# Kernel tuning notes

Measured on AMD Instinct MI355X. Metric: run time of the kernel, lower is better.

The kernel has to match this reference:

```python
import jax, jax.numpy as jnp
import numpy as np

H = 512      # hidden_size
GH = 512     # global_hidden_size
V = 128      # VOCAB_SIZE (one-hot arg_hot width)
D = 14       # tree depth; complete binary tree
NUM_OPS = 36
N_INT = 5    # num_internal_ops
N_NODES = 2 ** (D + 1) - 1  # 32767, heap layout: node i has children 2i+1, 2i+2


def _p(key, i, shape, s=0.05):
    return jax.random.normal(jax.random.fold_in(key, i), shape, dtype=jnp.float32) * s


def setup_inputs() -> dict:
    key = jax.random.key(0)
    return {
        "tokens": jax.random.randint(jax.random.fold_in(key, 0), (N_NODES,), 0, V),
        "validity_mask": jnp.ones((NUM_OPS,), jnp.float32),
        # binary tree-LSTM (blstm): 2 children
        "W_iou_b": _p(key, 1, (V, 3 * H)), "U_iou_b": _p(key, 2, (2, H, 3 * H)), "b_iou_b": jnp.zeros((3 * H,), jnp.float32),
        "Wf_b": _p(key, 3, (V, H)), "Uf_b": _p(key, 4, (2, H, H)), "bf_b": jnp.ones((H,), jnp.float32),
        # ternary tree-LSTM (tlstm): 3 children
        "W_iou_t": _p(key, 5, (V, 3 * H)), "U_iou_t": _p(key, 6, (3, H, 3 * H)), "b_iou_t": jnp.zeros((3 * H,), jnp.float32),
        "Wf_t": _p(key, 7, (V, H)), "Uf_t": _p(key, 8, (3, H, H)), "bf_t": jnp.ones((H,), jnp.float32),
        # FFN: one h-by-h layer (ffn_complexity = h^2 * n_layers, n_layers=1)
        "ffn_W": _p(key, 9, (H, H)), "ffn_b": jnp.zeros((H,), jnp.float32),
        # global LSTM (1 layer, 1 step), torch gate order i,f,g,o
        "lstm_Wx": _p(key, 10, (H, 4 * GH)), "lstm_Wh": _p(key, 11, (GH, 4 * GH)), "lstm_b": jnp.zeros((4 * GH,), jnp.float32),
        # actor heads on concat(root_hidden, h_glob)
        "hl_W": _p(key, 12, (H + GH, 2)), "hl_b": jnp.zeros((2,), jnp.float32),
        "int_W": _p(key, 13, (H + GH, N_INT)), "int_b": jnp.zeros((N_INT,), jnp.float32),
        "act_W": _p(key, 14, (H + GH, NUM_OPS)), "act_b": jnp.zeros((NUM_OPS,), jnp.float32),
    }


def _nary_cell(x, hk, ck, W_iou, U_iou, b_iou, Wf, Uf, bf):
    # x: [n, V]; hk, ck: [n, K, H]  (K children)
    iou = x @ W_iou + jnp.einsum('nkh,khg->ng', hk, U_iou) + b_iou
    i, o, u = jnp.split(iou, 3, axis=-1)
    f = jax.nn.sigmoid((x @ Wf + bf)[:, None, :] + jnp.einsum('nkh,khg->nkg', hk, Uf))
    c = jax.nn.sigmoid(i) * jnp.tanh(u) + jnp.sum(f * ck, axis=1)
    h = jax.nn.sigmoid(o) * jnp.tanh(c)
    return h, c


def _forward(tokens, validity_mask, W_iou_b, U_iou_b, b_iou_b, Wf_b, Uf_b, bf_b,
             W_iou_t, U_iou_t, b_iou_t, Wf_t, Uf_t, bf_t, ffn_W, ffn_b,
             lstm_Wx, lstm_Wh, lstm_b, hl_W, hl_b, int_W, int_b, act_W, act_b):
    arg_hot = jax.nn.one_hot(tokens, V, dtype=jnp.float32)  # [N_NODES, V]
    h_prev = c_prev = None
    h_ab = c_ab = None
    # apply_binary_lstm over the whole tree, bottom-up, one batched cell per level
    for lvl in range(D, -1, -1):
        n = 2 ** lvl
        x = arg_hot[n - 1:2 * n - 1]  # level lvl occupies heap slots [2^l-1, 2^{l+1}-2]
        if h_prev is None:
            hk = jnp.zeros((n, 2, H), jnp.float32)  # leaves: tz children
            ck = hk
        else:
            hk = h_prev.reshape(n, 2, H)
            ck = c_prev.reshape(n, 2, H)
        h_prev, c_prev = _nary_cell(x, hk, ck, W_iou_b, U_iou_b, b_iou_b, Wf_b, Uf_b, bf_b)
        if lvl == 1:
            h_ab, c_ab = h_prev, c_prev  # root's children a, b
    # apply_ternary_lstm at depth 0: children = (self.hidden, a.hidden, b.hidden)
    hk3 = jnp.concatenate([h_prev, h_ab], axis=0)[None]  # [1, 3, H]
    ck3 = jnp.concatenate([c_prev, c_ab], axis=0)[None]
    h_root, c_root = _nary_cell(arg_hot[0:1], hk3, ck3, W_iou_t, U_iou_t, b_iou_t, Wf_t, Uf_t, bf_t)
    # apply_ffn (1 layer) then apply_global_lstm (single step from zero state)
    h_f = jnp.maximum(h_root @ ffn_W + ffn_b, 0.0)  # [1, H]
    h_g = jnp.zeros((1, GH), jnp.float32)
    c_g = h_g
    gates = h_f @ lstm_Wx + h_g @ lstm_Wh + lstm_b
    gi, gf, gg, go = jnp.split(gates, 4, axis=-1)
    c_g = jax.nn.sigmoid(gf) * c_g + jax.nn.sigmoid(gi) * jnp.tanh(gg)
    h_g = jax.nn.sigmoid(go) * jnp.tanh(c_g)
    # actor heads
    feat = jnp.concatenate([h_f, h_g], axis=-1)  # [1, H+GH]
    hl = feat @ hl_W + hl_b
    il = feat @ int_W + int_b
    el = jnp.log(validity_mask)[None, :] + feat @ (act_W * validity_mask[None, :]) + act_b * validity_mask
    return jnp.concatenate([hl, il, el], axis=-1)  # [1, 2 + N_INT + NUM_OPS]


def reference(tokens, validity_mask, W_iou_b, U_iou_b, b_iou_b, Wf_b, Uf_b, bf_b,
              W_iou_t, U_iou_t, b_iou_t, Wf_t, Uf_t, bf_t, ffn_W, ffn_b,
              lstm_Wx, lstm_Wh, lstm_b, hl_W, hl_b, int_W, int_b, act_W, act_b):
    return _forward(tokens, validity_mask, W_iou_b, U_iou_b, b_iou_b, Wf_b, Uf_b, bf_b,
                    W_iou_t, U_iou_t, b_iou_t, Wf_t, Uf_t, bf_t, ffn_W, ffn_b,
                    lstm_Wx, lstm_Wh, lstm_b, hl_W, hl_b, int_W, int_b, act_W, act_b)
```

## Files before the change

### kernel.cpp

```cpp
#include <hip/hip_runtime.h>
#include <hip/hip_bf16.h>
#include <math.h>

#define H 512
#define V 128
#define NLEAF 16384

typedef __attribute__((ext_vector_type(4))) float f32x4;
typedef __attribute__((ext_vector_type(8))) short s16x8;
typedef __attribute__((ext_vector_type(4))) unsigned short u16x4;
typedef unsigned short ushort_t;

__device__ ushort_t g_hb0[NLEAF * H];
__device__ ushort_t g_hb1[(NLEAF / 2) * H];
__device__ float    g_c0[NLEAF * H];
__device__ float    g_c1[(NLEAF / 2) * H];
__device__ __align__(16) ushort_t g_htab[V * H];
__device__ __align__(16) float    g_ctab[V * H];
__device__ __align__(16) float    g_Wpack[V * H * 4];
__device__ __align__(16) float    g_Uh0[V * 3 * H];
__device__ __align__(16) float    g_Uh1[V * 3 * H];
__device__ __align__(16) float    g_Vf0[V * H];
__device__ __align__(16) float    g_Vf1[V * H];
__device__ __align__(16) float    g_uhp[4 * 2 * V * 2048];
__device__ ushort_t g_UiouT[3 * H * 2 * H];
__device__ ushort_t g_UfT[H * 2 * H];
__device__ ushort_t g_UiouTt[3 * H * 3 * H];
__device__ ushort_t g_UfTt[H * 3 * H];
__device__ float    g_rpart[3 * 3072];
__device__ float    g_hf[H];
__device__ float    g_gates[4 * H];

__device__ __forceinline__ float sigm(float x) { return 1.0f / (1.0f + __expf(-x)); }
__device__ __forceinline__ float ftanh(float x) {
  return 1.0f - 2.0f / (__expf(2.0f * x) + 1.0f);
}
__device__ __forceinline__ ushort_t f2bf(float x) {
  __hip_bfloat16 b = __float2bfloat16(x);
  return *reinterpret_cast<ushort_t*>(&b);
}
__device__ __forceinline__ float bf2f(ushort_t u) {
  union { unsigned int i; float f; } v; v.i = ((unsigned int)u) << 16; return v.f;
}
__device__ __forceinline__ void gload_lds16(const void* g, void* l) {
  __builtin_amdgcn_global_load_lds(
      (const __attribute__((address_space(1))) unsigned int*)g,
      (__attribute__((address_space(3))) unsigned int*)l, 16, 0, 0);
}
#define WAITV(N) asm volatile("s_waitcnt vmcnt(" #N ")" ::: "memory")

__global__ __launch_bounds__(256) void k_prep(
    const float* __restrict__ s0, const float* __restrict__ s1,
    const float* __restrict__ s2, const float* __restrict__ s3,
    ushort_t* __restrict__ d0, ushort_t* __restrict__ d1,
    ushort_t* __restrict__ d2, ushort_t* __restrict__ d3,
    const float* __restrict__ Wiou, const float* __restrict__ biou,
    const float* __restrict__ Wf, const float* __restrict__ bf) {
  if (blockIdx.z == 4) {
    const int v = blockIdx.y * 48 + blockIdx.x;
    if (v >= V) return;
    for (int j = threadIdx.x; j < H; j += 256) {
      float wi = Wiou[(size_t)v * 1536 + j] + biou[j];
      float wo = Wiou[(size_t)v * 1536 + 512 + j] + biou[512 + j];
      float wu = Wiou[(size_t)v * 1536 + 1024 + j] + biou[1024 + j];
      float wf = Wf[(size_t)v * 512 + j] + bf[j];
      f32x4 wp = {wi, wo, wu, wf};
      *reinterpret_cast<f32x4*>(&g_Wpack[((size_t)v * 512 + j) * 4]) = wp;
      float c = sigm(wi) * ftanh(wu);
      float h = sigm(wo) * ftanh(c);
      g_htab[v * H + j] = f2bf(h);
      g_ctab[v * H + j] = c;
    }
    return;
  }
  const float* src; ushort_t* dst; int R, Cc;
  switch (blockIdx.z) {
    case 0: src = s0; dst = d0; R = 1024; Cc = 1536; break;
    case 1: src = s1; dst = d1; R = 1024; Cc = 512; break;
    case 2: src = s2; dst = d2; R = 1536; Cc = 1536; break;
    default: src = s3; dst = d3; R = 1536; Cc = 512; break;
  }
  int bc = blockIdx.x * 32, br = blockIdx.y * 32;
  if (bc >= Cc || br >= R) return;
  __shared__ float t[32][33];
  int tx = threadIdx.x & 31, ty = threadIdx.x >> 5;
  for (int rr = ty; rr < 32; rr += 8)
    t[rr][tx] = src[(size_t)(br + rr) * Cc + bc + tx];
  __syncthreads();
  for (int rr = ty; rr < 32; rr += 8)
    dst[(size_t)(bc + rr) * R + br + tx] = f2bf(t[tx][rr]);
}

__global__ __launch_bounds__(256) void k_uhg() {
  const int cb0 = blockIdx.x * 64;
  const int kh = blockIdx.y;
  const int kc = blockIdx.z;
  const int tid = threadIdx.x;
  const int lane = tid & 63;
  const int w = tid >> 6;
  const int wry = w >> 1;
  const int cx = w & 1;

  __shared__ f32x4 suv[3072];
  char* smem = (char*)suv;

  const unsigned kA = (unsigned)(kc * 256) + ((lane >> 4) * 16);
  const unsigned kB = (unsigned)(kh * 1024) + kA;
  #pragma unroll
  for (int uu = 0; uu < 3; ++uu) {
    int u = w * 3 + uu;
    const char* base;
    unsigned dstb;
    if (u < 8) {
      int row = u * 16 + (lane & 15);
      base = (const char*)g_htab + (size_t)row * 1024 + kA;
      dstb = (unsigned)u * 4096u;
    } else {
      int col = cb0 + (u - 8) * 16 + (lane & 15);
      const ushort_t* cp = (col < 1536) ? (g_UiouT + (size_t)col * 1024)
                                        : (g_UfT + (size_t)(col - 1536) * 1024);
      base = (const char*)cp + kB;
      dstb = 32768u + (unsigned)(u - 8) * 4096u;
    }
    #pragma unroll
    for (int kt = 0; kt < 4; ++kt)
      gload_lds16(base + kt * 64, smem + dstb + kt * 1024u);
  }
  WAITV(0);
  __syncthreads();

  f32x4 acc[4][2];
  #pragma unroll
  for (int a = 0; a < 4; ++a) { acc[a][0] = (f32x4){0,0,0,0}; acc[a][1] = (f32x4){0,0,0,0}; }

  #pragma unroll
  for (int kt = 0; kt < 4; ++kt) {
    const char* ab = smem + wry * 16384 + kt * 1024 + lane * 16;
    const char* bb = smem + 32768 + cx * 8192 + kt * 1024 + lane * 16;
    s16x8 b0 = *(const s16x8*)(bb);
    s16x8 b1 = *(const s16x8*)(bb + 4096);
    #pragma unroll
    for (int rtl = 0; rtl < 4; ++rtl) {
      s16x8 av = *(const s16x8*)(ab + rtl * 4096);
      acc[rtl][0] = __builtin_amdgcn_mfma_f32_16x16x32_bf16(av, b0, acc[rtl][0], 0, 0, 0);
      acc[rtl][1] = __builtin_amdgcn_mfma_f32_16x16x32_bf16(av, b1, acc[rtl][1], 0, 0, 0);
    }
  }

  float* outb = g_uhp + ((size_t)(kc * 2 + kh) * V) * 2048;
  #pragma unroll
  for (int rtl = 0; rtl < 4; ++rtl) {
    #pragma unroll
    for (int t = 0; t < 2; ++t) {
      int col = cb0 + cx * 32 + t * 16 + (lane & 15);
      int vb = wry * 64 + rtl * 16 + (lane >> 4) * 4;
      #pragma unroll
      for (int r = 0; r < 4; ++r)
        outb[(size_t)(vb + r) * 2048 + col] = acc[rtl][t][r];
    }
  }
}

__global__ __launch_bounds__(256) void k_uhred() {
  int e = blockIdx.x * 256 + threadIdx.x;
  float s = g_uhp[e] + g_uhp[524288 + e] + g_uhp[2 * 524288 + e]
          + g_uhp[3 * 524288 + e];
  int kh = e >> 18;
  int rem = e & 262143;
  int v = rem >> 11;
  int c = rem & 2047;
  if (c < 1536) (kh ? g_Uh1 : g_Uh0)[(size_t)v * 1536 + c] = s;
  else          (kh ? g_Vf1 : g_Vf0)[(size_t)v * 512 + (c - 1536)] = s;
}

__global__ __launch_bounds__(256) void k_top_cell(const int* __restrict__ tokens) {
  const int total = 8192 * 128;
  for (int q = blockIdx.x * 256 + threadIdx.x; q < total; q += gridDim.x * 256) {
    int i = q >> 7, jv = q & 127;
    int t0 = tokens[(NLEAF - 1) + 2 * i];
    int t1 = tokens[(NLEAF - 1) + 2 * i + 1];
    int tk = tokens[8191 + i];
    const f32x4* u0 = (const f32x4*)&g_Uh0[(size_t)t0 * 1536];
    const f32x4* u1 = (const f32x4*)&g_Uh1[(size_t)t1 * 1536];
    f32x4 ii = u0[jv] + u1[jv];
    f32x4 oo = u0[128 + jv] + u1[128 + jv];
    f32x4 uu = u0[256 + jv] + u1[256 + jv];
    f32x4 v0 = ((const f32x4*)&g_Vf0[(size_t)t0 * 512])[jv];
    f32x4 v1 = ((const f32x4*)&g_Vf1[(size_t)t1 * 512])[jv];
    f32x4 c0 = ((const f32x4*)&g_ctab[(size_t)t0 * 512])[jv];
    f32x4 c1 = ((const f32x4*)&g_ctab[(size_t)t1 * 512])[jv];
    const f32x4* wpp = (const f32x4*)g_Wpack + (size_t)tk * 512 + jv * 4;
    u16x4 hv; f32x4 cv;
    #pragma unroll
    for (int r = 0; r < 4; ++r) {
      f32x4 wp = wpp[r];
      float ig = ii[r] + wp[0];
      float og = oo[r] + wp[1];
      float ug = uu[r] + wp[2];
      float fp = wp[3];
      float cc = sigm(ig) * ftanh(ug) + sigm(fp + v0[r]) * c0[r]
               + sigm(fp + v1[r]) * c1[r];
      float hh = sigm(og) * ftanh(cc);
      cv[r] = cc;
      hv[r] = f2bf(hh);
    }
    *reinterpret_cast<u16x4*>(&g_hb1[(size_t)q * 4]) = hv;
    *reinterpret_cast<f32x4*>(&g_c1[(size_t)q * 4]) = cv;
  }
}

#define COMPUTE64(FA, S)                                                     \
  {                                                                          \
    const char* ab = smem + buf * 16384 + wry * 8192 + (S) * 1024 + lane * 16; \
    s16x8 a0 = *(const s16x8*)(ab);                                          \
    s16x8 a1 = *(const s16x8*)(ab + 2048);                                   \
    s16x8 a2 = *(const s16x8*)(ab + 4096);                                   \
    s16x8 a3 = *(const s16x8*)(ab + 6144);                                   \
    const char* bb = smem + 32768 + buf * 32768 + cx * 4096 + (S) * 1024 + lane * 16; \
    s16x8 b0 = *(const s16x8*)(bb);                                          \
    s16x8 b1 = *(const s16x8*)(bb + 2048);                                   \
    s16x8 b2 = *(const s16x8*)(bb + 8192);                                   \
    s16x8 b3 = *(const s16x8*)(bb + 10240);                                  \
    s16x8 b4 = *(const s16x8*)(bb + 16384);                                  \
    s16x8 b5 = *(const s16x8*)(bb + 18432);                                  \
    s16x8 b6 = *(const s16x8*)(bb + 24576);                                  \
    s16x8 b7 = *(const s16x8*)(bb + 26624);                                  \
    s16x8 aa[4] = {a0, a1, a2, a3};                                          \
    _Pragma("unroll")                                                        \
    for (int rtl = 0; rtl < 4; ++rtl) {                                      \
      acc[rtl][0] = __builtin_amdgcn_mfma_f32_16x16x32_bf16(aa[rtl], b0, acc[rtl][0], 0, 0, 0); \
      acc[rtl][1] = __builtin_amdgcn_mfma_f32_16x16x32_bf16(aa[rtl], b1, acc[rtl][1], 0, 0, 0); \
      acc[rtl][2] = __builtin_amdgcn_mfma_f32_16x16x32_bf16(aa[rtl], b2, acc[rtl][2], 0, 0, 0); \
      acc[rtl][3] = __builtin_amdgcn_mfma_f32_16x16x32_bf16(aa[rtl], b3, acc[rtl][3], 0, 0, 0); \
      acc[rtl][4] = __builtin_amdgcn_mfma_f32_16x16x32_bf16(aa[rtl], b4, acc[rtl][4], 0, 0, 0); \
      acc[rtl][5] = __builtin_amdgcn_mfma_f32_16x16x32_bf16(aa[rtl], b5, acc[rtl][5], 0, 0, 0); \
      acc[rtl][FA] = __builtin_amdgcn_mfma_f32_16x16x32_bf16(aa[rtl], b6, acc[rtl][FA], 0, 0, 0); \
      acc[rtl][FA + 1] = __builtin_amdgcn_mfma_f32_16x16x32_bf16(aa[rtl], b7, acc[rtl][FA + 1], 0, 0, 0); \
    }                                                                        \
  }

__global__ __launch_bounds__(256, 1) void k_mfma_rest(int lvl,
    const int* __restrict__ tokens) {
  const int n = 1 << lvl;
  const int node0 = n - 1;
  const int outp = lvl & 1;
  const ushort_t* __restrict__ hprev = outp ? g_hb0 : g_hb1;
  const float* __restrict__ cprev = outp ? g_c0 : g_c1;
  ushort_t* __restrict__ hout = outp ? g_hb1 : g_hb0;
  float* __restrict__ cout = outp ? g_c1 : g_c0;

  const int i0 = blockIdx.x * 128;
  const int j0 = blockIdx.y * 64;
  const int tid = threadIdx.x;
  const int lane = tid & 63;
  const int w = tid >> 6;
  const int wry = w >> 1;
  const int cx = w & 1;

  __shared__ f32x4 smemv[6144];
  char* smem = (char*)smemv;

  const char* gp[6];
  unsigned lb[6], lstr[6];
  {
    int kb = (lane >> 4) * 16;
    #pragma unroll
    for (int q = 0; q < 6; ++q) {
      int c = w * 6 + q;
      if (c < 8) {
        int row = i0 + c * 16 + (lane & 15);
        gp[q] = (const char*)hprev + (size_t)row * 2048 + kb;
        lb[q] = c * 2048u;
        lstr[q] = 16384u;
      } else {
        int ct = c - 8;
        int col = ct * 16 + (lane & 15);
        int g = col >> 6, jj = j0 + (col & 63);
        const ushort_t* Ub = (g < 3) ? (g_UiouT + (size_t)(g * 512 + jj) * 1024)
                                     : (g_UfT + (size_t)jj * 1024);
        gp[q] = (const char*)Ub + kb;
        lb[q] = 32768u + ct * 2048u;
        lstr[q] = 32768u;
      }
    }
  }

#define STAGE2(BUF)                                                          \
  {                                                                          \
    _Pragma("unroll")                                                        \
    for (int q = 0; q < 6; ++q) {                                            \
      gload_lds16(gp[q], smem + lb[q] + (unsigned)(BUF) * lstr[q]);          \
      gp[q] += 64;                                                           \
      gload_lds16(gp[q], smem + lb[q] + (unsigned)(BUF) * lstr[q] + 1024u);  \
      gp[q] += 64;                                                           \
    }                                                                        \
  }

  f32x4 acc[4][10];
  #pragma unroll
  for (int a = 0; a < 4; ++a)
    #pragma unroll
    for (int b = 0; b < 10; ++b) acc[a][b] = (f32x4){0.f, 0.f, 0.f, 0.f};

  STAGE2(0); STAGE2(1);
  int buf = 0;
  for (int ph = 0; ph < 8; ++ph) {
    WAITV(12);
    __builtin_amdgcn_s_barrier();
    COMPUTE64(6, 0);
    COMPUTE64(6, 1);
    __builtin_amdgcn_s_barrier();
    STAGE2(buf);
    buf ^= 1;
  }
  for (int ph = 8; ph < 14; ++ph) {
    WAITV(12);
    __builtin_amdgcn_s_barrier();
    COMPUTE64(8, 0);
    COMPUTE64(8, 1);
    __builtin_amdgcn_s_barrier();
    STAGE2(buf);
    buf ^= 1;
  }
  WAITV(12); __builtin_amdgcn_s_barrier();
  COMPUTE64(8, 0); COMPUTE64(8, 1);
  buf ^= 1;
  WAITV(0); __builtin_amdgcn_s_barrier();
  COMPUTE64(8, 0); COMPUTE64(8, 1);
#undef STAGE2

  const int node_c = lane >> 4;
  const int jl = lane & 15;
  #pragma unroll
  for (int t = 0; t < 2; ++t) {
    const int j = j0 + cx * 32 + t * 16 + jl;
    #pragma unroll
    for (int rtl = 0; rtl < 4; ++rtl) {
      f32x4 vi = acc[rtl][0 + t], vo = acc[rtl][2 + t], vu = acc[rtl][4 + t],
            v0 = acc[rtl][6 + t], v1 = acc[rtl][8 + t];
      const int ib = i0 + wry * 64 + rtl * 16 + node_c * 4;
      #pragma unroll
      for (int r = 0; r < 4; ++r) {
        int i = ib + r;
        int tok = tokens[node0 + i];
        f32x4 wp = ((const f32x4*)g_Wpack)[(size_t)tok * 512 + j];
        float ig = vi[r] + wp[0];
        float og = vo[r] + wp[1];
        float ug = vu[r] + wp[2];
        float fpre = wp[3];
        float cc = sigm(ig) * ftanh(ug)
                 + sigm(fpre + v0[r]) * cprev[(size_t)(2 * i) * 512 + j]
                 + sigm(fpre + v1[r]) * cprev[(size_t)(2 * i + 1) * 512 + j];
        float hh = sigm(og) * ftanh(cc);
        hout[(size_t)i * 512 + j] = f2bf(hh);
        cout[(size_t)i * 512 + j] = cc;
      }
    }
  }
}

__global__ __launch_bounds__(256) void k_small(int lvl,
    const int* __restrict__ tokens) {
  const int n = 1 << lvl;
  const int node0 = n - 1;
  const int outp = lvl & 1;
  const ushort_t* __restrict__ hprev = outp ? g_hb0 : g_hb1;
  const float* __restrict__ cprev = outp ? g_c0 : g_c1;
  ushort_t* __restrict__ hout = outp ? g_hb1 : g_hb0;
  float* __restrict__ cout = outp ? g_c1 : g_c0;

  const int i = blockIdx.y;
  const int j0 = blockIdx.x * 64;
  const int tid = threadIdx.x;
  const int g = tid >> 6;
  const int jc = tid & 63;
  const int jj = j0 + jc;

  __shared__ float hl[1024];
  __shared__ float exch[5][64];
  for (int t = tid; t < 1024; t += 256) hl[t] = bf2f(hprev[(size_t)i * 1024 + t]);
  __syncthreads();

  const ushort_t* col = (g < 3) ? (g_UiouT + (size_t)(g * 512 + jj) * 1024)
                                : (g_UfT + (size_t)jj * 1024);
  float a0 = 0.f, a1 = 0.f;
  #pragma unroll 4
  for (int k0 = 0; k0 < 512; k0 += 8) {
    s16x8 wv = *(const s16x8*)(col + k0);
    #pragma unroll
    for (int r = 0; r < 8; ++r) a0 += hl[k0 + r] * bf2f((ushort_t)wv[r]);
  }
  #pragma unroll 4
  for (int k0 = 512; k0 < 1024; k0 += 8) {
    s16x8 wv = *(const s16x8*)(col + k0);
    #pragma unroll
    for (int r = 0; r < 8; ++r) a1 += hl[k0 + r] * bf2f((ushort_t)wv[r]);
  }
  if (g < 3) exch[g][jc] = a0 + a1;
  else { exch[3][jc] = a0; exch[4][jc] = a1; }
  __syncthreads();

  if (tid < 64) {
    int j = j0 + tid;
    int tok = tokens[node0 + i];
    f32x4 wp = ((const f32x4*)g_Wpack)[(size_t)tok * 512 + j];
    float ig = exch[0][tid] + wp[0];
    float og = exch[1][tid] + wp[1];
    float ug = exch[2][tid] + wp[2];
    float fpre = wp[3];
    float cc = sigm(ig) * ftanh(ug)
             + sigm(fpre + exch[3][tid]) * cprev[(size_t)(2 * i) * 512 + j]
             + sigm(fpre + exch[4][tid]) * cprev[(size_t)(2 * i + 1) * 512 + j];
    float hh = sigm(og) * ftanh(cc);
    hout[(size_t)i * 512 + j] = f2bf(hh);
    cout[(size_t)i * 512 + j] = cc;
  }
}

__global__ __launch_bounds__(256) void k_root_p1() {
  const int by = blockIdx.y;
  const int tid = threadIdx.x;
  const int c = blockIdx.x * 256 + tid;

  __shared__ float hl[512];
  {
    int m0 = by * 512;
    #pragma unroll
    for (int q = 0; q < 2; ++q) {
      int t = tid + q * 256, m = m0 + t;
      hl[t] = (m < 512) ? bf2f(g_hb0[m]) : bf2f(g_hb1[m - 512]);
    }
  }
  __syncthreads();

  float acc = 0.f;
  const ushort_t* col = nullptr;
  if (c < 1536) {
    col = g_UiouTt + (size_t)c * 1536 + by * 512;
  } else {
    int v = c - 1536;
    if ((v >> 9) == by) col = g_UfTt + (size_t)(v & 511) * 1536 + by * 512;
  }
  if (col) {
    #pragma unroll 4
    for (int k0 = 0; k0 < 512; k0 += 8) {
      s16x8 wv = *(const s16x8*)(col + k0);
      #pragma unroll
      for (int r = 0; r < 8; ++r) acc += hl[k0 + r] * bf2f((ushort_t)wv[r]);
    }
  }
  g_rpart[(size_t)by * 3072 + c] = acc;
}

__global__ __launch_bounds__(512) void k_p2h1(const int* __restrict__ tokens,
    const float* __restrict__ Wiou_t, const float* __restrict__ biou_t,
    const float* __restrict__ Wf_t, const float* __restrict__ bf_t,
    const float* __restrict__ ffnW, const float* __restrict__ ffnb) {
  __shared__ float hroot[H];
  const int j = threadIdx.x;
  float ai = g_rpart[j] + g_rpart[3072 + j] + g_rpart[6144 + j];
  float ao = g_rpart[512 + j] + g_rpart[3072 + 512 + j] + g_rpart[6144 + 512 + j];
  float au = g_rpart[1024 + j] + g_rpart[3072 + 1024 + j] + g_rpart[6144 + 1024 + j];
  float f0 = g_rpart[1536 + j] + g_rpart[3072 + 1536 + j] + g_rpart[6144 + 1536 + j];
  float f1 = g_rpart[2048 + j] + g_rpart[3072 + 2048 + j] + g_rpart[6144 + 2048 + j];
  float f2 = g_rpart[2560 + j] + g_rpart[3072 + 2560 + j] + g_rpart[6144 + 2560 + j];

  int tok = tokens[0];
  float fpre = Wf_t[(size_t)tok * H + j] + bf_t[j];
  float ig = ai + Wiou_t[(size_t)tok * 3 * H + j] + biou_t[j];
  float og = ao + Wiou_t[(size_t)tok * 3 * H + H + j] + biou_t[H + j];
  float ug = au + Wiou_t[(size_t)tok * 3 * H + 2 * H + j] + biou_t[2 * H + j];
  float cc = sigm(ig) * ftanh(ug)
           + sigm(fpre + f0) * g_c0[j]
           + sigm(fpre + f1) * g_c1[j]
           + sigm(fpre + f2) * g_c1[H + j];
  hroot[j] = sigm(og) * ftanh(cc);
  __syncthreads();

  float acc = ffnb[j];
  #pragma unroll 8
  for (int m = 0; m < H; ++m) acc += hroot[m] * ffnW[m * H + j];
  g_hf[j] = fmaxf(acc, 0.0f);
}

__global__ __launch_bounds__(64) void k_head2(const float* __restrict__ Wx,
                                              const float* __restrict__ lb) {
  int idx = blockIdx.x * 64 + threadIdx.x;
  int region = idx >> 9;
  int j = idx & 511;
  int g2 = (region == 0) ? j : ((region == 1) ? 1024 + j : 1536 + j);
  float acc = lb[g2];
  #pragma unroll 8
  for (int m = 0; m < H; ++m) acc += g_hf[m] * Wx[m * 4 * H + g2];
  g_gates[g2] = acc;
}

__global__ __launch_bounds__(512) void k_head3(const float* __restrict__ vm,
    const float* __restrict__ hlW, const float* __restrict__ hlb,
    const float* __restrict__ intW, const float* __restrict__ intb,
    const float* __restrict__ actW, const float* __restrict__ actb,
    float* __restrict__ out) {
  __shared__ float feat[2 * H];
  int j = threadIdx.x;
  float ci = sigm(g_gates[j]) * ftanh(g_gates[2 * H + j]);
  float hg = sigm(g_gates[3 * H + j]) * ftanh(ci);
  feat[j] = g_hf[j];
  feat[H + j] = hg;
  __syncthreads();

  const int wv = threadIdx.x >> 6;
  const int lane = threadIdx.x & 63;
  for (int o = wv; o < 43; o += 8) {
    const float* Wc;
    int stride, colb;
    if (o < 2)       { Wc = hlW;  stride = 2;  colb = o; }
    else if (o < 7)  { Wc = intW; stride = 5;  colb = o - 2; }
    else             { Wc = actW; stride = 36; colb = o - 7; }
    float s = 0.f;
    #pragma unroll
    for (int q = 0; q < 16; ++q) {
      int m = lane + q * 64;
      s += feat[m] * Wc[(size_t)m * stride + colb];
    }
    #pragma unroll
    for (int d = 32; d >= 1; d >>= 1) s += __shfl_xor(s, d);
    if (lane == 0) {
      float res;
      if (o < 2)      res = s + hlb[o];
      else if (o < 7) res = s + intb[o - 2];
      else {
        int a = o - 7;
        float v = vm[a];
        res = __logf(v) + s * v + actb[a] * v;
      }
      out[o] = res;
    }
  }
}

extern "C" void kernel_launch(void* const* d_in, const int* in_sizes, int n_in,
                              void* d_out, int out_size, void* d_ws, size_t ws_size,
                              hipStream_t stream) {
  (void)in_sizes; (void)n_in; (void)d_ws; (void)ws_size; (void)out_size;
  const int* tokens   = (const int*)d_in[0];
  const float* vm     = (const float*)d_in[1];
  const float* Wiou_b = (const float*)d_in[2];
  const float* Uiou_b = (const float*)d_in[3];
  const float* biou_b = (const float*)d_in[4];
  const float* Wf_b   = (const float*)d_in[5];
  const float* Uf_b   = (const float*)d_in[6];
  const float* bf_b   = (const float*)d_in[7];
  const float* Wiou_t = (const float*)d_in[8];
  const float* Uiou_t = (const float*)d_in[9];
  const float* biou_t = (const float*)d_in[10];
  const float* Wf_t   = (const float*)d_in[11];
  const float* Uf_t   = (const float*)d_in[12];
  const float* bf_t   = (const float*)d_in[13];
  const float* ffnW   = (const float*)d_in[14];
  const float* ffnb   = (const float*)d_in[15];
  const float* lstmWx = (const float*)d_in[16];
  const float* lstmb  = (const float*)d_in[18];
  const float* hlW    = (const float*)d_in[19];
  const float* hlb    = (const float*)d_in[20];
  const float* intW   = (const float*)d_in[21];
  const float* intb   = (const float*)d_in[22];
  const float* actW   = (const float*)d_in[23];
  const float* actb   = (const float*)d_in[24];

  ushort_t* UiouT;  hipGetSymbolAddress((void**)&UiouT, HIP_SYMBOL(g_UiouT));
  ushort_t* UfT;    hipGetSymbolAddress((void**)&UfT, HIP_SYMBOL(g_UfT));
  ushort_t* UiouTt; hipGetSymbolAddress((void**)&UiouTt, HIP_SYMBOL(g_UiouTt));
  ushort_t* UfTt;   hipGetSymbolAddress((void**)&UfTt, HIP_SYMBOL(g_UfTt));

  k_prep<<<dim3(48, 48, 5), 256, 0, stream>>>(
      Uiou_b, Uf_b, Uiou_t, Uf_t, UiouT, UfT, UiouTt, UfTt,
      Wiou_b, biou_b, Wf_b, bf_b);

  k_uhg<<<dim3(32, 2, 4), 256, 0, stream>>>();
  k_uhred<<<2048, 256, 0, stream>>>();
  k_top_cell<<<2048, 256, 0, stream>>>(tokens);

  for (int lvl = 12; lvl >= 8; --lvl) {
    int gx = (1 << lvl) / 128;
    k_mfma_rest<<<dim3(gx, 8), 256, 0, stream>>>(lvl, tokens);
  }
  for (int lvl = 7; lvl >= 0; --lvl) {
    int n = 1 << lvl;
    k_small<<<dim3(8, n), 256, 0, stream>>>(lvl, tokens);
  }
  k_root_p1<<<dim3(12, 3), 256, 0, stream>>>();
  k_p2h1<<<1, 512, 0, stream>>>(tokens, Wiou_t, biou_t, Wf_t, bf_t, ffnW, ffnb);
  k_head2<<<24, 64, 0, stream>>>(lstmWx, lstmb);
  k_head3<<<1, 512, 0, stream>>>(vm, hlW, hlb, intW, intb, actW, actb, (float*)d_out);
}
```

Baseline: 607.6 us.

## Pre-pack U weights into MFMA staging layout and use wave-per-column GEMV reductions

Adds a k_packU kernel that converts the binary-cell U matrices to bf16 in a tile-contiguous layout matching the MFMA level kernel's LDS staging order. Each wave then reads contiguous 1 KB chunks instead of strided rows. k_small and k_root_p1 now assign one wave per output column, keep the hidden vector in registers, use coalesced 16-byte weight loads, and reduce with cross-lane shuffles, replacing per-thread column walks over shared memory. The cost is an extra prep launch and a larger global scratch buffer.

```diff
diff --git a/kernel.cpp b/kernel.cpp
--- a/kernel.cpp
+++ b/kernel.cpp
@@ -25,6 +25,7 @@
 __device__ __align__(16) float    g_uhp[4 * 2 * V * 2048];
 __device__ ushort_t g_UiouT[3 * H * 2 * H];
 __device__ ushort_t g_UfT[H * 2 * H];
+__device__ __align__(16) ushort_t g_Ustage[8 * 16 * 32 * 64 * 8];
 __device__ ushort_t g_UiouTt[3 * H * 3 * H];
 __device__ ushort_t g_UfTt[H * 3 * H];
 __device__ float    g_rpart[3 * 3072];
@@ -89,6 +90,31 @@
   __syncthreads();
   for (int rr = ty; rr < 32; rr += 8)
     dst[(size_t)(bc + rr) * R + br + tx] = f2bf(t[tx][rr]);
+}
+
+__global__ __launch_bounds__(256) void k_packU(const float* __restrict__ Uiou,
+                                               const float* __restrict__ Uf) {
+  const int jb = blockIdx.x;
+  const int ct = blockIdx.y;
+  const int kz = blockIdx.z;
+  const int t = threadIdx.x;
+  const int kt = kz * 4 + (t >> 6);
+  const int lane = t & 63;
+  const int colu = ct * 16 + (lane & 15);
+  const int g = colu >> 6;
+  const int jj = jb * 64 + (colu & 63);
+  const int kbase = kt * 32 + ((lane >> 4) << 3);
+  u16x4 v0, v1;
+  #pragma unroll
+  for (int r = 0; r < 8; ++r) {
+    int k = kbase + r;
+    float v = (g < 3) ? Uiou[(size_t)k * 1536 + g * 512 + jj]
+                      : Uf[(size_t)k * 512 + jj];
+    if (r < 4) v0[r] = f2bf(v); else v1[r - 4] = f2bf(v);
+  }
+  ushort_t* dst = g_Ustage + (((size_t)(jb * 16 + ct) * 32 + kt) * 64 + lane) * 8;
+  *reinterpret_cast<u16x4*>(dst) = v0;
+  *reinterpret_cast<u16x4*>(dst + 4) = v1;
 }
 
 __global__ __launch_bounds__(256) void k_uhg() {
@@ -261,7 +287,7 @@
   char* smem = (char*)smemv;
 
   const char* gp[6];
-  unsigned lb[6], lstr[6];
+  unsigned lb[6], lstr[6], off2[6], adv[6];
   {
     int kb = (lane >> 4) * 16;
     #pragma unroll
@@ -270,17 +296,13 @@
       if (c < 8) {
         int row = i0 + c * 16 + (lane & 15);
         gp[q] = (const char*)hprev + (size_t)row * 2048 + kb;
-        lb[q] = c * 2048u;
-        lstr[q] = 16384u;
+        lb[q] = c * 2048u; lstr[q] = 16384u; off2[q] = 64u; adv[q] = 128u;
       } else {
         int ct = c - 8;
-        int col = ct * 16 + (lane & 15);
-        int g = col >> 6, jj = j0 + (col & 63);
-        const ushort_t* Ub = (g < 3) ? (g_UiouT + (size_t)(g * 512 + jj) * 1024)
-                                     : (g_UfT + (size_t)jj * 1024);
-        gp[q] = (const char*)Ub + kb;
-        lb[q] = 32768u + ct * 2048u;
-        lstr[q] = 32768u;
+        gp[q] = (const char*)g_Ustage +
+                ((size_t)(blockIdx.y * 16 + ct) << 15) + lane * 16;
+        lb[q] = 32768u + ct * 2048u; lstr[q] = 32768u;
+        off2[q] = 1024u; adv[q] = 2048u;
       }
     }
   }
@@ -290,9 +312,9 @@
     _Pragma("unroll")                                                        \
     for (int q = 0; q < 6; ++q) {                                            \
       gload_lds16(gp[q], smem + lb[q] + (unsigned)(BUF) * lstr[q]);          \
-      gp[q] += 64;                                                           \
-      gload_lds16(gp[q], smem + lb[q] + (unsigned)(BUF) * lstr[q] + 1024u);  \
-      gp[q] += 64;                                                           \
+      gload_lds16(gp[q] + off2[q],                                           \
+                  smem + lb[q] + (unsigned)(BUF) * lstr[q] + 1024u);         \
+      gp[q] += adv[q];                                                       \
     }                                                                        \
   }
 
@@ -372,32 +394,47 @@
   const int i = blockIdx.y;
   const int j0 = blockIdx.x * 64;
   const int tid = threadIdx.x;
-  const int g = tid >> 6;
-  const int jc = tid & 63;
-  const int jj = j0 + jc;
-
-  __shared__ float hl[1024];
+  const int lane = tid & 63;
+  const int w = tid >> 6;
+
   __shared__ float exch[5][64];
-  for (int t = tid; t < 1024; t += 256) hl[t] = bf2f(hprev[(size_t)i * 1024 + t]);
-  __syncthreads();
-
-  const ushort_t* col = (g < 3) ? (g_UiouT + (size_t)(g * 512 + jj) * 1024)
-                                : (g_UfT + (size_t)jj * 1024);
-  float a0 = 0.f, a1 = 0.f;
-  #pragma unroll 4
-  for (int k0 = 0; k0 < 512; k0 += 8) {
-    s16x8 wv = *(const s16x8*)(col + k0);
-    #pragma unroll
-    for (int r = 0; r < 8; ++r) a0 += hl[k0 + r] * bf2f((ushort_t)wv[r]);
-  }
-  #pragma unroll 4
-  for (int k0 = 512; k0 < 1024; k0 += 8) {
-    s16x8 wv = *(const s16x8*)(col + k0);
-    #pragma unroll
-    for (int r = 0; r < 8; ++r) a1 += hl[k0 + r] * bf2f((ushort_t)wv[r]);
-  }
-  if (g < 3) exch[g][jc] = a0 + a1;
-  else { exch[3][jc] = a0; exch[4][jc] = a1; }
+
+  float hv[16];
+  {
+    const s16x8* hp = (const s16x8*)(hprev + (size_t)i * 1024 + lane * 16);
+    s16x8 h0 = hp[0], h1 = hp[1];
+    #pragma unroll
+    for (int r = 0; r < 8; ++r) {
+      hv[r] = bf2f((ushort_t)h0[r]);
+      hv[8 + r] = bf2f((ushort_t)h1[r]);
+    }
+  }
+
+  for (int u = w; u < 256; u += 4) {
+    int jc = u & 63, g = u >> 6, jj = j0 + jc;
+    const ushort_t* col = (g < 3) ? (g_UiouT + (size_t)(g * 512 + jj) * 1024)
+                                  : (g_UfT + (size_t)jj * 1024);
+    const s16x8* cp = (const s16x8*)(col + lane * 16);
+    s16x8 w0 = cp[0], w1 = cp[1];
+    float s = 0.f;
+    #pragma unroll
+    for (int r = 0; r < 8; ++r) {
+      s += bf2f((ushort_t)w0[r]) * hv[r];
+      s += bf2f((ushort_t)w1[r]) * hv[8 + r];
+    }
+    s += __shfl_xor(s, 1);
+    s += __shfl_xor(s, 2);
+    s += __shfl_xor(s, 4);
+    s += __shfl_xor(s, 8);
+    s += __shfl_xor(s, 16);
+    if (g < 3) {
+      s += __shfl_xor(s, 32);
+      if (lane == 0) exch[g][jc] = s;
+    } else {
+      if (lane == 0) exch[3][jc] = s;
+      if (lane == 32) exch[4][jc] = s;
+    }
+  }
   __syncthreads();
 
   if (tid < 64) {
@@ -420,36 +457,43 @@
 __global__ __launch_bounds__(256) void k_root_p1() {
   const int by = blockIdx.y;
   const int tid = threadIdx.x;
-  const int c = blockIdx.x * 256 + tid;
-
-  __shared__ float hl[512];
+  const int lane = tid & 63;
+  const int w = tid >> 6;
+  const int cbase = blockIdx.x * 256;
+
+  float hv[8];
   {
-    int m0 = by * 512;
-    #pragma unroll
-    for (int q = 0; q < 2; ++q) {
-      int t = tid + q * 256, m = m0 + t;
-      hl[t] = (m < 512) ? bf2f(g_hb0[m]) : bf2f(g_hb1[m - 512]);
-    }
-  }
-  __syncthreads();
-
-  float acc = 0.f;
-  const ushort_t* col = nullptr;
-  if (c < 1536) {
-    col = g_UiouTt + (size_t)c * 1536 + by * 512;
-  } else {
-    int v = c - 1536;
-    if ((v >> 9) == by) col = g_UfTt + (size_t)(v & 511) * 1536 + by * 512;
-  }
-  if (col) {
-    #pragma unroll 4
-    for (int k0 = 0; k0 < 512; k0 += 8) {
-      s16x8 wv = *(const s16x8*)(col + k0);
+    int m0 = by * 512 + lane * 8;
+    #pragma unroll
+    for (int r = 0; r < 8; ++r) {
+      int m = m0 + r;
+      hv[r] = (m < 512) ? bf2f(g_hb0[m]) : bf2f(g_hb1[m - 512]);
+    }
+  }
+
+  for (int u = w; u < 256; u += 4) {
+    int c = cbase + u;
+    const ushort_t* col = nullptr;
+    if (c < 1536) {
+      col = g_UiouTt + (size_t)c * 1536 + by * 512;
+    } else {
+      int v = c - 1536;
+      if ((v >> 9) == by) col = g_UfTt + (size_t)(v & 511) * 1536 + by * 512;
+    }
+    float s = 0.f;
+    if (col) {
+      s16x8 wv = *(const s16x8*)(col + lane * 8);
       #pragma unroll
-      for (int r = 0; r < 8; ++r) acc += hl[k0 + r] * bf2f((ushort_t)wv[r]);
-    }
-  }
-  g_rpart[(size_t)by * 3072 + c] = acc;
+      for (int r = 0; r < 8; ++r) s += bf2f((ushort_t)wv[r]) * hv[r];
+    }
+    s += __shfl_xor(s, 1);
+    s += __shfl_xor(s, 2);
+    s += __shfl_xor(s, 4);
+    s += __shfl_xor(s, 8);
+    s += __shfl_xor(s, 16);
+    s += __shfl_xor(s, 32);
+    if (lane == 0) g_rpart[(size_t)by * 3072 + c] = s;
+  }
 }
 
 __global__ __launch_bounds__(512) void k_p2h1(const int* __restrict__ tokens,
@@ -575,6 +619,7 @@
   k_prep<<<dim3(48, 48, 5), 256, 0, stream>>>(
       Uiou_b, Uf_b, Uiou_t, Uf_t, UiouT, UfT, UiouTt, UfTt,
       Wiou_b, biou_b, Wf_b, bf_b);
+  k_packU<<<dim3(8, 16, 8), 256, 0, stream>>>(Uiou_b, Uf_b);
 
   k_uhg<<<dim3(32, 2, 4), 256, 0, stream>>>();
   k_uhred<<<2048, 256, 0, stream>>>();
```

Result: slower. 685.3 us (+12.8%).
